# Kernel tuning notes

Hardware: AMD Instinct MI355X
Metric: run time of the kernel (lower is better)

The kernel has to match this reference:

```python
import jax, jax.numpy as jnp
import numpy as np

N_NODES = 50000
N_EDGES = 800000
D = 128


def _gcn_layer(h, src, dst, norm, W, b, n_nodes):
    # h: [N, Din]; linear transform first (PyG GCNConv does x @ W then propagate)
    h = h @ W  # [N, Dout]
    msg = h[src] * norm[:, None]  # gather + per-edge scale, [E+N, Dout]
    out = jax.ops.segment_sum(msg, dst, num_segments=n_nodes)  # scatter-add
    return out + b


def setup_inputs() -> dict:
    key = jax.random.key(0)
    k_x, k_e, k_w1, k_w2 = jax.random.split(key, 4)
    x = jax.random.normal(k_x, (N_NODES, D), dtype=jnp.float32)
    edge_index = jax.random.randint(k_e, (2, N_EDGES), 0, N_NODES, dtype=jnp.int64)
    # Glorot-ish init for GCN weights
    s = 1.0 / np.sqrt(D)
    W1 = jax.random.uniform(k_w1, (D, D), jnp.float32, -s, s)
    W2 = jax.random.uniform(k_w2, (D, D), jnp.float32, -s, s)
    b1 = jnp.zeros((D,), jnp.float32)
    b2 = jnp.zeros((D,), jnp.float32)
    return {"x": x, "edge_index": edge_index, "W1": W1, "b1": b1, "W2": W2, "b2": b2}


def reference(x, edge_index, W1, b1, W2, b2):
    n = x.shape[0]
    loop = jnp.arange(n, dtype=edge_index.dtype)
    # add self-loops (GCNConv default add_self_loops=True)
    src = jnp.concatenate([edge_index[0], loop])
    dst = jnp.concatenate([edge_index[1], loop])
    # symmetric normalization: deg counted at aggregation (dst) side
    deg = jax.ops.segment_sum(jnp.ones_like(src, dtype=x.dtype), dst, num_segments=n)
    dinv = jnp.where(deg > 0, jax.lax.rsqrt(deg), 0.0)
    norm = dinv[src] * dinv[dst]  # [E+N]
    h = jax.nn.relu(_gcn_layer(x, src, dst, norm, W1, b1, n))
    # F.dropout(p=0.2, training=False) -> identity in eval mode
    h = jax.nn.relu(_gcn_layer(h, src, dst, norm, W2, b2, n))
    return h
```

## Files before the change

### kernel.cpp

```cpp
#include <hip/hip_runtime.h>
#include <hip/hip_bf16.h>

typedef __hip_bfloat16 bf16h;
typedef short short8 __attribute__((ext_vector_type(8)));
typedef float floatx4 __attribute__((ext_vector_type(4)));

__device__ __forceinline__ float bfu2f(unsigned int u) {
    return __uint_as_float((u & 0xffffu) << 16);
}
__device__ __forceinline__ float bfhi2f(unsigned int u) {
    return __uint_as_float(u & 0xffff0000u);
}
__device__ __forceinline__ unsigned short f2bfu(float f) {
    bf16h b = __float2bfloat16(f);
    return *(unsigned short*)&b;
}

#define SLOTS 64

__global__ __launch_bounds__(256) void k_prep(const void* __restrict__ x,
                                              const void* __restrict__ W1, const void* __restrict__ b1,
                                              const void* __restrict__ W2, const void* __restrict__ b2,
                                              int* __restrict__ cnt,
                                              unsigned short* __restrict__ W1h, unsigned short* __restrict__ W1l,
                                              unsigned short* __restrict__ W2h, unsigned short* __restrict__ W2l,
                                              float* __restrict__ bfv1, float* __restrict__ bfv2,
                                              unsigned int* __restrict__ Xb, int n) {
    int t = threadIdx.x;
    __shared__ int sIsB;
    if (t < 64) {
        unsigned int w = ((const unsigned int*)x)[t];
        unsigned int ef = (w >> 7) & 0xFFu;
        unsigned long long b = __ballot(ef >= 0x76u && ef <= 0x82u);
        if (t == 0) sIsB = (__popcll(b) >= 40) ? 1 : 0;
    }
    __syncthreads();
    bool isb = sIsB != 0;

    int gsz = gridDim.x * 256;
    int gid = blockIdx.x * 256 + t;
    for (int i = gid; i < n; i += gsz) cnt[i] = 0;
    for (int i = gid; i < 16384; i += gsz) {
        int c  = i >> 11;
        int kk = (i >> 9) & 3;
        int ln = (i >> 3) & 63;
        int j  = i & 7;
        int k    = kk * 32 + (ln >> 4) * 8 + j;
        int ncol = c * 16 + (ln & 15);
        int src  = k * 128 + ncol;
        float v1 = isb ? bfu2f(((const unsigned short*)W1)[src]) : ((const float*)W1)[src];
        float v2 = isb ? bfu2f(((const unsigned short*)W2)[src]) : ((const float*)W2)[src];
        unsigned short h1 = f2bfu(v1), h2 = f2bfu(v2);
        W1h[i] = h1; W1l[i] = f2bfu(v1 - bfu2f(h1));
        W2h[i] = h2; W2l[i] = f2bfu(v2 - bfu2f(h2));
    }
    if (gid < 128) {
        bfv1[gid] = isb ? bfu2f(((const unsigned short*)b1)[gid]) : ((const float*)b1)[gid];
        bfv2[gid] = isb ? bfu2f(((const unsigned short*)b2)[gid]) : ((const float*)b2)[gid];
    }
    int total = n * 64;
    if (isb) {
        const unsigned int* xs = (const unsigned int*)x;
        for (int i = gid; i < total; i += gsz) Xb[i] = xs[i];
    } else {
        const float2* xf = (const float2*)x;
        for (int i = gid; i < total; i += gsz) {
            float2 v = xf[i];
            Xb[i] = ((unsigned int)f2bfu(v.y) << 16) | f2bfu(v.x);
        }
    }
}

__global__ __launch_bounds__(256) void k_countfill(const int* __restrict__ ei,
                                                   int* __restrict__ cnt,
                                                   int* __restrict__ slots,
                                                   int e, int n, int rpx) {
    __shared__ int sSt;
    int t = threadIdx.x;
    if (t < 64) {
        int v = ei[2 * t + 1];
        unsigned long long b = __ballot(v == 0);
        if (t == 0) sSt = (b == ~0ull) ? 2 : 1;
    }
    __syncthreads();
    int st = sSt;
    int xcd = blockIdx.x & 7;
    int i = (blockIdx.x >> 3) * 256 + t;
    if (i >= e) return;
    int d = ei[(size_t)e * st + (size_t)i * st];
    int lo = xcd * rpx, hi = min(n, lo + rpx);
    if (d < lo || d >= hi) return;
    int s = ei[(size_t)i * st];
    if (s < 0 || s >= n) return;
    int pos = atomicAdd(&cnt[d], 1);
    if (pos < SLOTS) slots[(size_t)d * SLOTS + pos] = s;
}

template <bool OUT_BF16>
__global__ __launch_bounds__(256) void k_fused(const unsigned int* __restrict__ Xt,
                                               const int* __restrict__ cnt,
                                               const int* __restrict__ slots,
                                               const unsigned short* __restrict__ Wh,
                                               const unsigned short* __restrict__ Wl,
                                               const float* __restrict__ bias,
                                               void* __restrict__ out, int n) {
    __shared__ float sA[16][132];
    int t = threadIdx.x;
    int wv = t >> 6, lane = t & 63;
    int g = lane >> 4, l = lane & 15;
    int col = l * 4;
    int rowBase = blockIdx.x * 16;
    int nm1 = n - 1;

    int i = wv * 4 + g;
    int node = rowBase + i;
    int nodeC = min(node, nm1);
    int deg = (node < n) ? cnt[nodeC] : 0;
    int end = min(deg, SLOTS);
    const int* sl = slots + (size_t)nodeC * SLOTS;
    float acc[8] = {0.f, 0.f, 0.f, 0.f, 0.f, 0.f, 0.f, 0.f};
    int4 sv = *(const int4*)(sl);
    for (int j = 0; j < end; j += 4) {
        int4 cur = sv;
        if (j + 4 < end) sv = *(const int4*)(sl + j + 4);
        int ss[4] = {cur.x, cur.y, cur.z, cur.w};
#pragma unroll
        for (int k = 0; k < 4; ++k) {
            bool ok = (j + k) < end;
            int s = ok ? ss[k] : nodeC;
            float w = ok ? rsqrtf((float)cnt[s] + 1.0f) : 0.f;
            uint4 v = *(const uint4*)(Xt + (size_t)s * 64 + col);
            acc[0] += w * bfu2f(v.x);  acc[1] += w * bfhi2f(v.x);
            acc[2] += w * bfu2f(v.y);  acc[3] += w * bfhi2f(v.y);
            acc[4] += w * bfu2f(v.z);  acc[5] += w * bfhi2f(v.z);
            acc[6] += w * bfu2f(v.w);  acc[7] += w * bfhi2f(v.w);
        }
    }
    {
        float wd = rsqrtf((float)deg + 1.0f);
        uint4 v = *(const uint4*)(Xt + (size_t)nodeC * 64 + col);
        acc[0] += wd * bfu2f(v.x);  acc[1] += wd * bfhi2f(v.x);
        acc[2] += wd * bfu2f(v.y);  acc[3] += wd * bfhi2f(v.y);
        acc[4] += wd * bfu2f(v.z);  acc[5] += wd * bfhi2f(v.z);
        acc[6] += wd * bfu2f(v.w);  acc[7] += wd * bfhi2f(v.w);
        float* po = &sA[i][l * 8];
#pragma unroll
        for (int q = 0; q < 8; ++q) po[q] = wd * acc[q];
    }
    __syncthreads();

    floatx4 acc2[2];
    acc2[0] = (floatx4){0.f, 0.f, 0.f, 0.f};
    acc2[1] = (floatx4){0.f, 0.f, 0.f, 0.f};

#pragma unroll
    for (int kk = 0; kk < 4; ++kk) {
        const float* ap = &sA[l][kk * 32 + g * 8];
        float av[8];
#pragma unroll
        for (int j2 = 0; j2 < 8; ++j2) av[j2] = ap[j2];
        short8 ah, alo;
#pragma unroll
        for (int j2 = 0; j2 < 8; ++j2) {
            unsigned short h = f2bfu(av[j2]);
            ah[j2]  = (short)h;
            alo[j2] = (short)f2bfu(av[j2] - bfu2f(h));
        }
#pragma unroll
        for (int cc = 0; cc < 2; ++cc) {
            int c = wv * 2 + cc;
            int fo = ((c * 4 + kk) * 64 + lane) * 8;
            short8 bh = *(const short8*)(Wh + fo);
            short8 bl = *(const short8*)(Wl + fo);
            acc2[cc] = __builtin_amdgcn_mfma_f32_16x16x32_bf16(ah, bh, acc2[cc], 0, 0, 0);
            acc2[cc] = __builtin_amdgcn_mfma_f32_16x16x32_bf16(alo, bh, acc2[cc], 0, 0, 0);
            acc2[cc] = __builtin_amdgcn_mfma_f32_16x16x32_bf16(ah, bl, acc2[cc], 0, 0, 0);
        }
    }

#pragma unroll
    for (int cc = 0; cc < 2; ++cc) {
        int c = wv * 2 + cc;
        int ncol = c * 16 + l;
        float bv = bias[ncol];
#pragma unroll
        for (int r = 0; r < 4; ++r) {
            int row = rowBase + g * 4 + r;
            if (row < n) {
                float o = fmaxf(acc2[cc][r] + bv, 0.f);
                if constexpr (OUT_BF16) {
                    ((unsigned short*)out)[(size_t)row * 128 + ncol] = f2bfu(o);
                } else {
                    ((float*)out)[(size_t)row * 128 + ncol] = o;
                }
            }
        }
    }
}

extern "C" void kernel_launch(void* const* d_in, const int* in_sizes, int n_in,
                              void* d_out, int out_size, void* d_ws, size_t ws_size,
                              hipStream_t stream) {
    const int n = in_sizes[0] / 128;
    const int e = in_sizes[1] / 2;
    const void* x = d_in[0];
    const int* ei = (const int*)d_in[1];

    char* w = (char*)d_ws;
    size_t o = 0;
    auto alloc = [&](size_t bytes) -> char* {
        char* p = w + o;
        o += (bytes + 255) & ~(size_t)255;
        return p;
    };
    int* cnt   = (int*)alloc((size_t)n * 4);
    int* slots = (int*)alloc((size_t)n * SLOTS * 4 + 16);
    unsigned short* W1h = (unsigned short*)alloc(16384 * 2);
    unsigned short* W1l = (unsigned short*)alloc(16384 * 2);
    unsigned short* W2h = (unsigned short*)alloc(16384 * 2);
    unsigned short* W2l = (unsigned short*)alloc(16384 * 2);
    float* bf1 = (float*)alloc(128 * 4);
    float* bf2 = (float*)alloc(128 * 4);
    unsigned int* Xb  = (unsigned int*)alloc((size_t)n * 64 * 4);
    unsigned int* Xb2 = (unsigned int*)alloc((size_t)n * 64 * 4);
    (void)ws_size;

    k_prep<<<1024, 256, 0, stream>>>(x, d_in[2], d_in[3], d_in[4], d_in[5],
                                     cnt, W1h, W1l, W2h, W2l, bf1, bf2, Xb, n);
    const int rpx = (n + 7) / 8;
    int ecx = ((e + 255) / 256) * 8;
    k_countfill<<<ecx, 256, 0, stream>>>(ei, cnt, slots, e, n, rpx);

    int gf = (n + 15) / 16;
    k_fused<true><<<gf, 256, 0, stream>>>(Xb, cnt, slots, W1h, W1l, bf1, Xb2, n);
    k_fused<false><<<gf, 256, 0, stream>>>(Xb2, cnt, slots, W2h, W2l, bf2, d_out, n);
}
```

Measured before the change: 229.6 us.

## Precompute dinv, process 32 rows per block, unroll gather by 8

Adds a small kernel that computes each node's inverse-sqrt degree once, so the fused kernels load it instead of computing rsqrt from cnt on every edge. Each fused block now aggregates 32 nodes in two halves and runs the MFMA transform twice, which halves the grid and reuses the weight fragments across more rows. The neighbour loop loads 8 slot indices at a time for more memory-level parallelism, and gather addresses use 32-bit offsets. The cost is one extra launch, twice the shared memory per block, and more register pressure.

```diff
diff --git a/kernel.cpp b/kernel.cpp
--- a/kernel.cpp
+++ b/kernel.cpp
@@ -96,102 +96,119 @@
     if (pos < SLOTS) slots[(size_t)d * SLOTS + pos] = s;
 }
 
+__global__ __launch_bounds__(256) void k_dinv(const int* __restrict__ cnt,
+                                              float* __restrict__ dinv, int n) {
+    int i = blockIdx.x * 256 + threadIdx.x;
+    if (i < n) dinv[i] = rsqrtf((float)cnt[i] + 1.0f);
+}
+
 template <bool OUT_BF16>
 __global__ __launch_bounds__(256) void k_fused(const unsigned int* __restrict__ Xt,
                                                const int* __restrict__ cnt,
+                                               const float* __restrict__ dinv,
                                                const int* __restrict__ slots,
                                                const unsigned short* __restrict__ Wh,
                                                const unsigned short* __restrict__ Wl,
                                                const float* __restrict__ bias,
                                                void* __restrict__ out, int n) {
-    __shared__ float sA[16][132];
+    __shared__ float sA[32][132];
     int t = threadIdx.x;
     int wv = t >> 6, lane = t & 63;
     int g = lane >> 4, l = lane & 15;
     int col = l * 4;
-    int rowBase = blockIdx.x * 16;
+    int rowBase = blockIdx.x * 32;
     int nm1 = n - 1;
-
-    int i = wv * 4 + g;
-    int node = rowBase + i;
-    int nodeC = min(node, nm1);
-    int deg = (node < n) ? cnt[nodeC] : 0;
-    int end = min(deg, SLOTS);
-    const int* sl = slots + (size_t)nodeC * SLOTS;
-    float acc[8] = {0.f, 0.f, 0.f, 0.f, 0.f, 0.f, 0.f, 0.f};
-    int4 sv = *(const int4*)(sl);
-    for (int j = 0; j < end; j += 4) {
-        int4 cur = sv;
-        if (j + 4 < end) sv = *(const int4*)(sl + j + 4);
-        int ss[4] = {cur.x, cur.y, cur.z, cur.w};
-#pragma unroll
-        for (int k = 0; k < 4; ++k) {
-            bool ok = (j + k) < end;
-            int s = ok ? ss[k] : nodeC;
-            float w = ok ? rsqrtf((float)cnt[s] + 1.0f) : 0.f;
-            uint4 v = *(const uint4*)(Xt + (size_t)s * 64 + col);
-            acc[0] += w * bfu2f(v.x);  acc[1] += w * bfhi2f(v.x);
-            acc[2] += w * bfu2f(v.y);  acc[3] += w * bfhi2f(v.y);
-            acc[4] += w * bfu2f(v.z);  acc[5] += w * bfhi2f(v.z);
-            acc[6] += w * bfu2f(v.w);  acc[7] += w * bfhi2f(v.w);
-        }
-    }
-    {
-        float wd = rsqrtf((float)deg + 1.0f);
-        uint4 v = *(const uint4*)(Xt + (size_t)nodeC * 64 + col);
-        acc[0] += wd * bfu2f(v.x);  acc[1] += wd * bfhi2f(v.x);
-        acc[2] += wd * bfu2f(v.y);  acc[3] += wd * bfhi2f(v.y);
-        acc[4] += wd * bfu2f(v.z);  acc[5] += wd * bfhi2f(v.z);
-        acc[6] += wd * bfu2f(v.w);  acc[7] += wd * bfhi2f(v.w);
-        float* po = &sA[i][l * 8];
-#pragma unroll
-        for (int q = 0; q < 8; ++q) po[q] = wd * acc[q];
+    int grp = wv * 4 + g;
+
+#pragma unroll
+    for (int half = 0; half < 2; ++half) {
+        int i = half * 16 + grp;
+        int node = rowBase + i;
+        int nodeC = min(node, nm1);
+        int end = (node < n) ? min(cnt[nodeC], SLOTS) : 0;
+        const int* sl = slots + (size_t)nodeC * SLOTS;
+        float acc[8] = {0.f, 0.f, 0.f, 0.f, 0.f, 0.f, 0.f, 0.f};
+        int4 sva = *(const int4*)(sl);
+        int4 svb = *(const int4*)(sl + 4);
+        for (int j = 0; j < end; j += 8) {
+            int4 ca = sva, cb = svb;
+            if (j + 8 < end) {
+                sva = *(const int4*)(sl + j + 8);
+                svb = *(const int4*)(sl + j + 12);
+            }
+            int ss[8] = {ca.x, ca.y, ca.z, ca.w, cb.x, cb.y, cb.z, cb.w};
+#pragma unroll
+            for (int k = 0; k < 8; ++k) {
+                bool ok = (j + k) < end;
+                int s = ok ? ss[k] : nodeC;
+                float w = ok ? dinv[s] : 0.f;
+                uint4 v = *(const uint4*)(Xt + (unsigned)(s * 64 + col));
+                acc[0] += w * bfu2f(v.x);  acc[1] += w * bfhi2f(v.x);
+                acc[2] += w * bfu2f(v.y);  acc[3] += w * bfhi2f(v.y);
+                acc[4] += w * bfu2f(v.z);  acc[5] += w * bfhi2f(v.z);
+                acc[6] += w * bfu2f(v.w);  acc[7] += w * bfhi2f(v.w);
+            }
+        }
+        {
+            float wd = dinv[nodeC];
+            uint4 v = *(const uint4*)(Xt + (unsigned)(nodeC * 64 + col));
+            acc[0] += wd * bfu2f(v.x);  acc[1] += wd * bfhi2f(v.x);
+            acc[2] += wd * bfu2f(v.y);  acc[3] += wd * bfhi2f(v.y);
+            acc[4] += wd * bfu2f(v.z);  acc[5] += wd * bfhi2f(v.z);
+            acc[6] += wd * bfu2f(v.w);  acc[7] += wd * bfhi2f(v.w);
+            float* po = &sA[i][l * 8];
+#pragma unroll
+            for (int q = 0; q < 8; ++q) po[q] = wd * acc[q];
+        }
     }
     __syncthreads();
 
-    floatx4 acc2[2];
-    acc2[0] = (floatx4){0.f, 0.f, 0.f, 0.f};
-    acc2[1] = (floatx4){0.f, 0.f, 0.f, 0.f};
-
-#pragma unroll
-    for (int kk = 0; kk < 4; ++kk) {
-        const float* ap = &sA[l][kk * 32 + g * 8];
-        float av[8];
-#pragma unroll
-        for (int j2 = 0; j2 < 8; ++j2) av[j2] = ap[j2];
-        short8 ah, alo;
-#pragma unroll
-        for (int j2 = 0; j2 < 8; ++j2) {
-            unsigned short h = f2bfu(av[j2]);
-            ah[j2]  = (short)h;
-            alo[j2] = (short)f2bfu(av[j2] - bfu2f(h));
-        }
+#pragma unroll
+    for (int tau = 0; tau < 2; ++tau) {
+        floatx4 acc2[2];
+        acc2[0] = (floatx4){0.f, 0.f, 0.f, 0.f};
+        acc2[1] = (floatx4){0.f, 0.f, 0.f, 0.f};
+
+#pragma unroll
+        for (int kk = 0; kk < 4; ++kk) {
+            const float* ap = &sA[tau * 16 + l][kk * 32 + g * 8];
+            float av[8];
+#pragma unroll
+            for (int j2 = 0; j2 < 8; ++j2) av[j2] = ap[j2];
+            short8 ah, alo;
+#pragma unroll
+            for (int j2 = 0; j2 < 8; ++j2) {
+                unsigned short h = f2bfu(av[j2]);
+                ah[j2]  = (short)h;
+                alo[j2] = (short)f2bfu(av[j2] - bfu2f(h));
+            }
+#pragma unroll
+            for (int cc = 0; cc < 2; ++cc) {
+                int c = wv * 2 + cc;
+                int fo = ((c * 4 + kk) * 64 + lane) * 8;
+                short8 bh = *(const short8*)(Wh + fo);
+                short8 bl = *(const short8*)(Wl + fo);
+                acc2[cc] = __builtin_amdgcn_mfma_f32_16x16x32_bf16(ah, bh, acc2[cc], 0, 0, 0);
+                acc2[cc] = __builtin_amdgcn_mfma_f32_16x16x32_bf16(alo, bh, acc2[cc], 0, 0, 0);
+                acc2[cc] = __builtin_amdgcn_mfma_f32_16x16x32_bf16(ah, bl, acc2[cc], 0, 0, 0);
+            }
+        }
+
 #pragma unroll
         for (int cc = 0; cc < 2; ++cc) {
             int c = wv * 2 + cc;
-            int fo = ((c * 4 + kk) * 64 + lane) * 8;
-            short8 bh = *(const short8*)(Wh + fo);
-            short8 bl = *(const short8*)(Wl + fo);
-            acc2[cc] = __builtin_amdgcn_mfma_f32_16x16x32_bf16(ah, bh, acc2[cc], 0, 0, 0);
-            acc2[cc] = __builtin_amdgcn_mfma_f32_16x16x32_bf16(alo, bh, acc2[cc], 0, 0, 0);
-            acc2[cc] = __builtin_amdgcn_mfma_f32_16x16x32_bf16(ah, bl, acc2[cc], 0, 0, 0);
-        }
-    }
-
-#pragma unroll
-    for (int cc = 0; cc < 2; ++cc) {
-        int c = wv * 2 + cc;
-        int ncol = c * 16 + l;
-        float bv = bias[ncol];
-#pragma unroll
-        for (int r = 0; r < 4; ++r) {
-            int row = rowBase + g * 4 + r;
-            if (row < n) {
-                float o = fmaxf(acc2[cc][r] + bv, 0.f);
-                if constexpr (OUT_BF16) {
-                    ((unsigned short*)out)[(size_t)row * 128 + ncol] = f2bfu(o);
-                } else {
-                    ((float*)out)[(size_t)row * 128 + ncol] = o;
+            int ncol = c * 16 + l;
+            float bv = bias[ncol];
+#pragma unroll
+            for (int r = 0; r < 4; ++r) {
+                int row = rowBase + tau * 16 + g * 4 + r;
+                if (row < n) {
+                    float o = fmaxf(acc2[cc][r] + bv, 0.f);
+                    if constexpr (OUT_BF16) {
+                        ((unsigned short*)out)[(size_t)row * 128 + ncol] = f2bfu(o);
+                    } else {
+                        ((float*)out)[(size_t)row * 128 + ncol] = o;
+                    }
                 }
             }
         }
@@ -214,7 +231,8 @@
         return p;
     };
     int* cnt   = (int*)alloc((size_t)n * 4);
-    int* slots = (int*)alloc((size_t)n * SLOTS * 4 + 16);
+    float* dinv = (float*)alloc((size_t)n * 4);
+    int* slots = (int*)alloc((size_t)n * SLOTS * 4 + 64);
     unsigned short* W1h = (unsigned short*)alloc(16384 * 2);
     unsigned short* W1l = (unsigned short*)alloc(16384 * 2);
     unsigned short* W2h = (unsigned short*)alloc(16384 * 2);
@@ -230,8 +248,9 @@
     const int rpx = (n + 7) / 8;
     int ecx = ((e + 255) / 256) * 8;
     k_countfill<<<ecx, 256, 0, stream>>>(ei, cnt, slots, e, n, rpx);
-
-    int gf = (n + 15) / 16;
-    k_fused<true><<<gf, 256, 0, stream>>>(Xb, cnt, slots, W1h, W1l, bf1, Xb2, n);
-    k_fused<false><<<gf, 256, 0, stream>>>(Xb2, cnt, slots, W2h, W2l, bf2, d_out, n);
-}
+    k_dinv<<<(n + 255) / 256, 256, 0, stream>>>(cnt, dinv, n);
+
+    int gf = (n + 31) / 32;
+    k_fused<true><<<gf, 256, 0, stream>>>(Xb, cnt, dinv, slots, W1h, W1l, bf1, Xb2, n);
+    k_fused<false><<<gf, 256, 0, stream>>>(Xb2, cnt, dinv, slots, W2h, W2l, bf2, d_out, n);
+}
```

New measurement: 208.3 us. -9.3%, faster.
